# Kernel optimization log

Measured on AMD Instinct MI355X. Metric: run time of the kernel, lower is better.

Reference implementation:

```python
import jax, jax.numpy as jnp
import numpy as np

D_MODEL = 1024
NUM_HEADS = 16
HEAD_DIM = D_MODEL // NUM_HEADS
B, S = 2, 2048


def setup_inputs() -> dict:
    key = jax.random.key(0)
    ks = jax.random.split(key, 6)
    scale = 0.02
    return {
        "x": jax.random.normal(ks[0], (B, S, D_MODEL), dtype=jnp.float32),
        "mask": jax.random.normal(ks[1], (S, S), dtype=jnp.float32),
        "Wqkv": jax.random.normal(ks[2], (D_MODEL, 3 * D_MODEL), dtype=jnp.float32) * scale,
        "bqkv": jax.random.normal(ks[3], (3 * D_MODEL,), dtype=jnp.float32) * scale,
        "Wout": jax.random.normal(ks[4], (D_MODEL, D_MODEL), dtype=jnp.float32) * scale,
        "bout": jax.random.normal(ks[5], (D_MODEL,), dtype=jnp.float32) * scale,
    }


def reference(x, mask, Wqkv, bqkv, Wout, bout):
    b, s, d = x.shape
    h, hd = NUM_HEADS, HEAD_DIM
    qkv = x @ Wqkv + bqkv                              # [b, s, 3d]
    qkv = qkv.reshape(b, s, h, 3 * hd).transpose(0, 2, 1, 3)  # [b, h, s, 3hd]
    q, k, v = jnp.split(qkv, 3, axis=-1)               # each [b, h, s, hd]
    scaled = jnp.einsum("bhqd,bhkd->bhqk", q, k) / jnp.sqrt(jnp.float32(hd))
    scaled = scaled + mask                             # mask [s, s] broadcasts
    attn = jax.nn.softmax(scaled, axis=-1)
    values = jnp.einsum("bhqk,bhkd->bhqd", attn, v)    # [b, h, s, hd]
    values = values.transpose(0, 2, 1, 3).reshape(b, s, d)
    return values @ Wout + bout
```

## Files before the change

kernel.cpp:

```cpp
#include <hip/hip_runtime.h>
#include <hip/hip_bf16.h>

#define D_MODEL 1024
#define NH 16
#define HD 64
#define BATCH 2
#define SEQ 2048
#define M_TOTAL (BATCH*SEQ)

typedef _Float16 f16;
typedef _Float16 half8 __attribute__((ext_vector_type(8)));
typedef _Float16 half4v __attribute__((ext_vector_type(4)));
typedef float floatx4 __attribute__((ext_vector_type(4)));

__device__ inline void gload_lds16(const void* g, void* l) {
    __builtin_amdgcn_global_load_lds(
        (const __attribute__((address_space(1))) unsigned int*)g,
        (__attribute__((address_space(3))) unsigned int*)l, 16, 0, 0);
}

__global__ void cvt_f32_f16(const float* __restrict__ src, f16* __restrict__ dst, int n4) {
    int i = blockIdx.x * blockDim.x + threadIdx.x;
    if (i < n4) {
        float4 v = ((const float4*)src)[i];
        half4v o = { (f16)v.x, (f16)v.y, (f16)v.z, (f16)v.w };
        *(half4v*)(dst + (long)i * 4) = o;
    }
}

__global__ void exp_cvt(const float* __restrict__ src, f16* __restrict__ dst, int n4) {
    int i = blockIdx.x * blockDim.x + threadIdx.x;
    if (i < n4) {
        float4 v = ((const float4*)src)[i];
        half4v o = { (f16)__expf(v.x), (f16)__expf(v.y), (f16)__expf(v.z), (f16)__expf(v.w) };
        *(half4v*)(dst + (long)i * 4) = o;
    }
}

__global__ void transpose_cvt(const float* __restrict__ src, f16* __restrict__ dst, int R, int C) {
    __shared__ float tile[32][33];
    int tx = threadIdx.x;
    int ty = threadIdx.y;
    int c0 = blockIdx.x * 32;
    int r0 = blockIdx.y * 32;
    for (int yy = 0; yy < 32; yy += 8)
        tile[ty + yy][tx] = src[(long)(r0 + ty + yy) * C + c0 + tx];
    __syncthreads();
    for (int yy = 0; yy < 32; yy += 8)
        dst[(long)(c0 + ty + yy) * R + r0 + tx] = (f16)tile[tx][ty + yy];
}

template<int MODE, int TN>
__global__ __launch_bounds__(256) void gemm_mfma(
    const f16* __restrict__ A, const f16* __restrict__ BT,
    const float* __restrict__ bias,
    f16* __restrict__ Qh, f16* __restrict__ Kh, f16* __restrict__ Vtg,
    float* __restrict__ out, int Kdim)
{
    constexpr int NF = TN / 32;
    __shared__ f16 Ah[128 * 64];
    __shared__ f16 Bh[TN * 64];
    int tid  = threadIdx.x;
    int wid  = tid >> 6;
    int lane = tid & 63;
    int quad = lane >> 4;
    int l16  = lane & 15;
    int m0 = blockIdx.y * 128;
    int n0 = blockIdx.x * TN;
    int mrow = (wid >> 1) * 64;
    int ncol = (wid & 1) * (TN / 2);
    int grow = lane >> 3;
    int gchunk = (lane & 7) ^ (grow & 7);
    int sw0 = ((quad)     ^ (l16 & 7)) * 8;
    int sw1 = ((quad + 4) ^ (l16 & 7)) * 8;

    floatx4 acc[4][NF];
    #pragma unroll
    for (int mb = 0; mb < 4; mb++)
        #pragma unroll
        for (int nb = 0; nb < NF; nb++) acc[mb][nb] = (floatx4){0.f, 0.f, 0.f, 0.f};

    const f16* Abase = A + (long)m0 * Kdim;
    const f16* Bbase = BT + (long)n0 * Kdim;

    for (int k0 = 0; k0 < Kdim; k0 += 64) {
        #pragma unroll
        for (int j = 0; j < 4; j++) {
            int r = j * 32 + wid * 8 + grow;
            gload_lds16(Abase + (long)r * Kdim + k0 + gchunk * 8, &Ah[(j * 32 + wid * 8) * 64]);
        }
        #pragma unroll
        for (int j = 0; j < TN / 32; j++) {
            int r = j * 32 + wid * 8 + grow;
            gload_lds16(Bbase + (long)r * Kdim + k0 + gchunk * 8, &Bh[(j * 32 + wid * 8) * 64]);
        }
        __syncthreads();
        #pragma unroll
        for (int h = 0; h < 2; h++) {
            int sw = h ? sw1 : sw0;
            half8 af[4];
            #pragma unroll
            for (int mb = 0; mb < 4; mb++)
                af[mb] = *(const half8*)&Ah[(mrow + mb * 16 + l16) * 64 + sw];
            #pragma unroll
            for (int nb = 0; nb < NF; nb++) {
                half8 bf = *(const half8*)&Bh[(ncol + nb * 16 + l16) * 64 + sw];
                #pragma unroll
                for (int mb = 0; mb < 4; mb++)
                    acc[mb][nb] = __builtin_amdgcn_mfma_f32_16x16x32_f16(af[mb], bf, acc[mb][nb], 0, 0, 0);
            }
        }
        __syncthreads();
    }

    #pragma unroll
    for (int nb = 0; nb < NF; nb++) {
        int n = n0 + ncol + nb * 16 + l16;
        float bv = bias[n];
        int head = 0, t = 0, d = 0;
        if (MODE == 0) { head = n / 192; int rem = n % 192; t = rem / 64; d = rem % 64; }
        #pragma unroll
        for (int mb = 0; mb < 4; mb++) {
            int mbase = m0 + mrow + mb * 16 + quad * 4;
            if (MODE == 0) {
                int b = mbase >> 11;
                int s = mbase & 2047;
                long bh = b * NH + head;
                if (t == 2) {
                    half4v pack;
                    #pragma unroll
                    for (int r = 0; r < 4; r++) pack[r] = (f16)(acc[mb][nb][r] + bv);
                    *(half4v*)&Vtg[(bh * HD + d) * SEQ + s] = pack;
                } else if (t == 0) {
                    #pragma unroll
                    for (int r = 0; r < 4; r++)
                        Qh[(bh * SEQ + s + r) * HD + d] = (f16)((acc[mb][nb][r] + bv) * 0.125f);
                } else {
                    #pragma unroll
                    for (int r = 0; r < 4; r++)
                        Kh[(bh * SEQ + s + r) * HD + d] = (f16)(acc[mb][nb][r] + bv);
                }
            } else {
                #pragma unroll
                for (int r = 0; r < 4; r++)
                    out[(long)(mbase + r) * D_MODEL + n] = acc[mb][nb][r] + bv;
            }
        }
    }
}

__global__ __launch_bounds__(256) void attn(
    const f16* __restrict__ Qh, const f16* __restrict__ Kh, const f16* __restrict__ Vtg,
    const f16* __restrict__ E, f16* __restrict__ valh)
{
    __shared__ f16 Kl[2][64 * 64];
    __shared__ f16 Vt[2][64 * 64];
    int tid  = threadIdx.x;
    int wid  = tid >> 6;
    int lane = tid & 63;
    int quad = lane >> 4;
    int l16  = lane & 15;
    int bh = blockIdx.y;
    int b  = bh >> 4;
    int h  = bh & 15;
    int q0 = blockIdx.x * 128 + wid * 32;

    int grow = lane >> 3;
    int gpos = lane & 7;
    int l3   = l16 & 7;
    int sw0 = ((quad)     ^ l3) * 8;
    int sw1 = ((quad + 4) ^ l3) * 8;
    int qh  = quad >> 1;
    int ql4 = (quad & 1) * 4;

    const f16* Qbase = Qh + ((long)bh * SEQ + q0) * HD;
    half8 qf[2][2];
    #pragma unroll
    for (int m = 0; m < 2; m++)
        #pragma unroll
        for (int c = 0; c < 2; c++)
            qf[m][c] = *(const half8*)&Qbase[(long)(m * 16 + l16) * HD + c * 32 + quad * 8];

    floatx4 Of[2][4];
    float sums[2] = {0.f, 0.f};
    #pragma unroll
    for (int m = 0; m < 2; m++)
        #pragma unroll
        for (int nb = 0; nb < 4; nb++) Of[m][nb] = (floatx4){0.f, 0.f, 0.f, 0.f};

    const f16* Kb = Kh + (long)bh * SEQ * HD;
    const f16* Vb = Vtg + (long)bh * HD * SEQ;

    #pragma unroll
    for (int j = 0; j < 2; j++) {
        int rb = j * 32 + wid * 8;
        int row = rb + grow;
        int gk = gpos ^ (row & 7);
        gload_lds16(Kb + (long)row * HD + gk * 8, &Kl[0][rb * 64]);
        gload_lds16(Vb + (long)row * SEQ + gk * 8, &Vt[0][rb * 64]);
    }

    half4v ef[2][2][4];
    #pragma unroll
    for (int m = 0; m < 2; m++)
        #pragma unroll
        for (int kb = 0; kb < 4; kb++)
            ef[0][m][kb] = *(const half4v*)&E[(long)(q0 + m * 16 + l16) * SEQ + kb * 16 + quad * 4];

    for (int it2 = 0; it2 < SEQ / 128; it2++) {
        #pragma unroll
        for (int p = 0; p < 2; p++) {
            int k0 = it2 * 128 + p * 64;
            __syncthreads();

            if (k0 + 64 < SEQ) {
                int kn = k0 + 64;
                #pragma unroll
                for (int j = 0; j < 2; j++) {
                    int rb = j * 32 + wid * 8;
                    int row = rb + grow;
                    int gk = gpos ^ (row & 7);
                    gload_lds16(Kb + (long)(kn + row) * HD + gk * 8, &Kl[p ^ 1][rb * 64]);
                    gload_lds16(Vb + (long)row * SEQ + kn + gk * 8, &Vt[p ^ 1][rb * 64]);
                }
                #pragma unroll
                for (int m = 0; m < 2; m++)
                    #pragma unroll
                    for (int kb = 0; kb < 4; kb++)
                        ef[p ^ 1][m][kb] = *(const half4v*)&E[(long)(q0 + m * 16 + l16) * SEQ + kn + kb * 16 + quad * 4];
            }

            half4v ph[2][4];
            #pragma unroll
            for (int kb = 0; kb < 4; kb++) {
                half8 kf0 = *(const half8*)&Kl[p][(kb * 16 + l16) * 64 + sw0];
                half8 kf1 = *(const half8*)&Kl[p][(kb * 16 + l16) * 64 + sw1];
                #pragma unroll
                for (int m = 0; m < 2; m++) {
                    floatx4 s = (floatx4){0.f, 0.f, 0.f, 0.f};
                    s = __builtin_amdgcn_mfma_f32_16x16x32_f16(kf0, qf[m][0], s, 0, 0, 0);
                    s = __builtin_amdgcn_mfma_f32_16x16x32_f16(kf1, qf[m][1], s, 0, 0, 0);
                    #pragma unroll
                    for (int r = 0; r < 4; r++) {
                        float pv = (float)ef[p][m][kb][r] * __expf(s[r]);
                        sums[m] += pv;
                        ph[m][kb][r] = (f16)pv;
                    }
                }
            }

            #pragma unroll
            for (int kb = 0; kb < 4; kb++) {
                int chunk = ((kb * 2 + qh) ^ l3) * 8 + ql4;
                #pragma unroll
                for (int nb = 0; nb < 4; nb++) {
                    half4v vf = *(const half4v*)&Vt[p][(nb * 16 + l16) * 64 + chunk];
                    #pragma unroll
                    for (int m = 0; m < 2; m++)
                        Of[m][nb] = __builtin_amdgcn_mfma_f32_16x16x16f16(vf, ph[m][kb], Of[m][nb], 0, 0, 0);
                }
            }
        }
    }

    #pragma unroll
    for (int m = 0; m < 2; m++) {
        float s = sums[m];
        s += __shfl_xor(s, 16);
        s += __shfl_xor(s, 32);
        sums[m] = 1.f / s;
    }

    #pragma unroll
    for (int m = 0; m < 2; m++) {
        long row = (long)(b * SEQ + q0 + m * 16 + l16) * D_MODEL + h * HD;
        #pragma unroll
        for (int nb = 0; nb < 4; nb++) {
            half4v o;
            #pragma unroll
            for (int r = 0; r < 4; r++) o[r] = (f16)(Of[m][nb][r] * sums[m]);
            *(half4v*)&valh[row + nb * 16 + quad * 4] = o;
        }
    }
}

extern "C" void kernel_launch(void* const* d_in, const int* in_sizes, int n_in,
                              void* d_out, int out_size, void* d_ws, size_t ws_size,
                              hipStream_t stream) {
    const float* x    = (const float*)d_in[0];
    const float* mask = (const float*)d_in[1];
    const float* Wqkv = (const float*)d_in[2];
    const float* bqkv = (const float*)d_in[3];
    const float* Wout = (const float*)d_in[4];
    const float* bout = (const float*)d_in[5];
    float* out = (float*)d_out;

    char* ws = (char*)d_ws;
    f16* xh    = (f16*)(ws + 0);
    f16* E     = (f16*)(ws + 0);
    f16* WqkvT = (f16*)(ws + 8388608);
    f16* WoutT = (f16*)(ws + 14680064);
    f16* Qh    = (f16*)(ws + 16777216);
    f16* Kh    = (f16*)(ws + 25165824);
    f16* Vtg   = (f16*)(ws + 33554432);
    f16* valh  = (f16*)(ws + 41943040);

    cvt_f32_f16<<<4096, 256, 0, stream>>>(x, xh, M_TOTAL * D_MODEL / 4);
    transpose_cvt<<<dim3(96, 32), dim3(32, 8), 0, stream>>>(Wqkv, WqkvT, 1024, 3072);
    transpose_cvt<<<dim3(32, 32), dim3(32, 8), 0, stream>>>(Wout, WoutT, 1024, 1024);
    gemm_mfma<0, 128><<<dim3(24, 32), 256, 0, stream>>>(xh, WqkvT, bqkv, Qh, Kh, Vtg, nullptr, 1024);
    exp_cvt<<<4096, 256, 0, stream>>>(mask, E, SEQ * SEQ / 4);
    attn<<<dim3(16, 32), 256, 0, stream>>>(Qh, Kh, Vtg, E, valh);
    gemm_mfma<1, 64><<<dim3(16, 32), 256, 0, stream>>>(valh, WoutT, bout, nullptr, nullptr, nullptr, out, 1024);
}
```

Measured before the change: 243.3 us.

## Shrink attention blocks, use exp2 with folded scale, MFMA row sums

The attention kernel now runs 128-thread blocks over 64 queries with a single K/V LDS buffer, which doubles the grid and raises occupancy. Softmax exponentials use exp2 with log2e folded into the Q scaling. Probabilities are converted and multiplied by the exp-mask in packed fp16. Row sums come from an extra MFMA against a ones vector instead of per-lane adds and shuffles. The double-buffered prefetch of K/V is lost, so load latency must now be hidden by having more resident blocks.

```diff
diff --git a/kernel.cpp b/kernel.cpp
--- a/kernel.cpp
+++ b/kernel.cpp
@@ -11,12 +11,19 @@
 typedef _Float16 f16;
 typedef _Float16 half8 __attribute__((ext_vector_type(8)));
 typedef _Float16 half4v __attribute__((ext_vector_type(4)));
+typedef _Float16 half2v __attribute__((ext_vector_type(2)));
+typedef __fp16 fp16x2 __attribute__((ext_vector_type(2)));
 typedef float floatx4 __attribute__((ext_vector_type(4)));
 
 __device__ inline void gload_lds16(const void* g, void* l) {
     __builtin_amdgcn_global_load_lds(
         (const __attribute__((address_space(1))) unsigned int*)g,
         (__attribute__((address_space(3))) unsigned int*)l, 16, 0, 0);
+}
+
+__device__ inline half2v pack_f16(float a, float b) {
+    fp16x2 t = __builtin_amdgcn_cvt_pkrtz(a, b);
+    return __builtin_bit_cast(half2v, t);
 }
 
 __global__ void cvt_f32_f16(const float* __restrict__ src, f16* __restrict__ dst, int n4) {
@@ -134,7 +141,7 @@
                 } else if (t == 0) {
                     #pragma unroll
                     for (int r = 0; r < 4; r++)
-                        Qh[(bh * SEQ + s + r) * HD + d] = (f16)((acc[mb][nb][r] + bv) * 0.125f);
+                        Qh[(bh * SEQ + s + r) * HD + d] = (f16)((acc[mb][nb][r] + bv) * 0.1803368801f);
                 } else {
                     #pragma unroll
                     for (int r = 0; r < 4; r++)
@@ -149,12 +156,12 @@
     }
 }
 
-__global__ __launch_bounds__(256) void attn(
+__global__ __launch_bounds__(128, 4) void attn(
     const f16* __restrict__ Qh, const f16* __restrict__ Kh, const f16* __restrict__ Vtg,
     const f16* __restrict__ E, f16* __restrict__ valh)
 {
-    __shared__ f16 Kl[2][64 * 64];
-    __shared__ f16 Vt[2][64 * 64];
+    __shared__ f16 Kl[64 * 64];
+    __shared__ f16 Vt[64 * 64];
     int tid  = threadIdx.x;
     int wid  = tid >> 6;
     int lane = tid & 63;
@@ -163,7 +170,7 @@
     int bh = blockIdx.y;
     int b  = bh >> 4;
     int h  = bh & 15;
-    int q0 = blockIdx.x * 128 + wid * 32;
+    int q0 = blockIdx.x * 64 + wid * 32;
 
     int grow = lane >> 3;
     int gpos = lane & 7;
@@ -181,72 +188,80 @@
         for (int c = 0; c < 2; c++)
             qf[m][c] = *(const half8*)&Qbase[(long)(m * 16 + l16) * HD + c * 32 + quad * 8];
 
+    half4v vones;
+    #pragma unroll
+    for (int j = 0; j < 4; j++) vones[j] = (f16)1.0f;
+
     floatx4 Of[2][4];
-    float sums[2] = {0.f, 0.f};
-    #pragma unroll
-    for (int m = 0; m < 2; m++)
+    floatx4 Ofs[2];
+    #pragma unroll
+    for (int m = 0; m < 2; m++) {
+        Ofs[m] = (floatx4){0.f, 0.f, 0.f, 0.f};
         #pragma unroll
         for (int nb = 0; nb < 4; nb++) Of[m][nb] = (floatx4){0.f, 0.f, 0.f, 0.f};
+    }
 
     const f16* Kb = Kh + (long)bh * SEQ * HD;
     const f16* Vb = Vtg + (long)bh * HD * SEQ;
-
-    #pragma unroll
-    for (int j = 0; j < 2; j++) {
-        int rb = j * 32 + wid * 8;
-        int row = rb + grow;
-        int gk = gpos ^ (row & 7);
-        gload_lds16(Kb + (long)row * HD + gk * 8, &Kl[0][rb * 64]);
-        gload_lds16(Vb + (long)row * SEQ + gk * 8, &Vt[0][rb * 64]);
-    }
+    const f16* Erow0 = E + (long)(q0 + l16) * SEQ + quad * 4;
+    const f16* Erow1 = E + (long)(q0 + 16 + l16) * SEQ + quad * 4;
 
     half4v ef[2][2][4];
     #pragma unroll
-    for (int m = 0; m < 2; m++)
-        #pragma unroll
-        for (int kb = 0; kb < 4; kb++)
-            ef[0][m][kb] = *(const half4v*)&E[(long)(q0 + m * 16 + l16) * SEQ + kb * 16 + quad * 4];
+    for (int kb = 0; kb < 4; kb++) {
+        ef[0][0][kb] = *(const half4v*)&Erow0[kb * 16];
+        ef[0][1][kb] = *(const half4v*)&Erow1[kb * 16];
+    }
 
     for (int it2 = 0; it2 < SEQ / 128; it2++) {
         #pragma unroll
         for (int p = 0; p < 2; p++) {
-            int k0 = it2 * 128 + p * 64;
+            int k0 = (it2 * 2 + p) * 64;
+            __syncthreads();
+            #pragma unroll
+            for (int j = 0; j < 4; j++) {
+                int rb = wid * 32 + j * 8;
+                int row = rb + grow;
+                int gk = gpos ^ grow;
+                gload_lds16(Kb + (long)(k0 + row) * HD + gk * 8, &Kl[rb * 64]);
+                gload_lds16(Vb + (long)row * SEQ + k0 + gk * 8, &Vt[rb * 64]);
+            }
             __syncthreads();
 
             if (k0 + 64 < SEQ) {
                 int kn = k0 + 64;
                 #pragma unroll
-                for (int j = 0; j < 2; j++) {
-                    int rb = j * 32 + wid * 8;
-                    int row = rb + grow;
-                    int gk = gpos ^ (row & 7);
-                    gload_lds16(Kb + (long)(kn + row) * HD + gk * 8, &Kl[p ^ 1][rb * 64]);
-                    gload_lds16(Vb + (long)row * SEQ + kn + gk * 8, &Vt[p ^ 1][rb * 64]);
+                for (int kb = 0; kb < 4; kb++) {
+                    ef[p ^ 1][0][kb] = *(const half4v*)&Erow0[kn + kb * 16];
+                    ef[p ^ 1][1][kb] = *(const half4v*)&Erow1[kn + kb * 16];
                 }
-                #pragma unroll
-                for (int m = 0; m < 2; m++)
-                    #pragma unroll
-                    for (int kb = 0; kb < 4; kb++)
-                        ef[p ^ 1][m][kb] = *(const half4v*)&E[(long)(q0 + m * 16 + l16) * SEQ + kn + kb * 16 + quad * 4];
             }
 
             half4v ph[2][4];
             #pragma unroll
             for (int kb = 0; kb < 4; kb++) {
-                half8 kf0 = *(const half8*)&Kl[p][(kb * 16 + l16) * 64 + sw0];
-                half8 kf1 = *(const half8*)&Kl[p][(kb * 16 + l16) * 64 + sw1];
+                half8 kf0 = *(const half8*)&Kl[(kb * 16 + l16) * 64 + sw0];
+                half8 kf1 = *(const half8*)&Kl[(kb * 16 + l16) * 64 + sw1];
                 #pragma unroll
                 for (int m = 0; m < 2; m++) {
                     floatx4 s = (floatx4){0.f, 0.f, 0.f, 0.f};
                     s = __builtin_amdgcn_mfma_f32_16x16x32_f16(kf0, qf[m][0], s, 0, 0, 0);
                     s = __builtin_amdgcn_mfma_f32_16x16x32_f16(kf1, qf[m][1], s, 0, 0, 0);
-                    #pragma unroll
-                    for (int r = 0; r < 4; r++) {
-                        float pv = (float)ef[p][m][kb][r] * __expf(s[r]);
-                        sums[m] += pv;
-                        ph[m][kb][r] = (f16)pv;
-                    }
+                    half2v lo = pack_f16(__builtin_amdgcn_exp2f(s[0]), __builtin_amdgcn_exp2f(s[1]));
+                    half2v hi = pack_f16(__builtin_amdgcn_exp2f(s[2]), __builtin_amdgcn_exp2f(s[3]));
+                    half2v el = { ef[p][m][kb][0], ef[p][m][kb][1] };
+                    half2v eh = { ef[p][m][kb][2], ef[p][m][kb][3] };
+                    lo *= el;
+                    hi *= eh;
+                    half4v pp = { lo[0], lo[1], hi[0], hi[1] };
+                    ph[m][kb] = pp;
                 }
+            }
+
+            #pragma unroll
+            for (int kb = 0; kb < 4; kb++) {
+                Ofs[0] = __builtin_amdgcn_mfma_f32_16x16x16f16(vones, ph[0][kb], Ofs[0], 0, 0, 0);
+                Ofs[1] = __builtin_amdgcn_mfma_f32_16x16x16f16(vones, ph[1][kb], Ofs[1], 0, 0, 0);
             }
 
             #pragma unroll
@@ -254,7 +269,7 @@
                 int chunk = ((kb * 2 + qh) ^ l3) * 8 + ql4;
                 #pragma unroll
                 for (int nb = 0; nb < 4; nb++) {
-                    half4v vf = *(const half4v*)&Vt[p][(nb * 16 + l16) * 64 + chunk];
+                    half4v vf = *(const half4v*)&Vt[(nb * 16 + l16) * 64 + chunk];
                     #pragma unroll
                     for (int m = 0; m < 2; m++)
                         Of[m][nb] = __builtin_amdgcn_mfma_f32_16x16x16f16(vf, ph[m][kb], Of[m][nb], 0, 0, 0);
@@ -263,13 +278,9 @@
         }
     }
 
-    #pragma unroll
-    for (int m = 0; m < 2; m++) {
-        float s = sums[m];
-        s += __shfl_xor(s, 16);
-        s += __shfl_xor(s, 32);
-        sums[m] = 1.f / s;
-    }
+    float rs[2];
+    #pragma unroll
+    for (int m = 0; m < 2; m++) rs[m] = 1.f / Ofs[m][0];
 
     #pragma unroll
     for (int m = 0; m < 2; m++) {
@@ -278,7 +289,7 @@
         for (int nb = 0; nb < 4; nb++) {
             half4v o;
             #pragma unroll
-            for (int r = 0; r < 4; r++) o[r] = (f16)(Of[m][nb][r] * sums[m]);
+            for (int r = 0; r < 4; r++) o[r] = (f16)(Of[m][nb][r] * rs[m]);
             *(half4v*)&valh[row + nb * 16 + quad * 4] = o;
         }
     }
@@ -310,6 +321,6 @@
     transpose_cvt<<<dim3(32, 32), dim3(32, 8), 0, stream>>>(Wout, WoutT, 1024, 1024);
     gemm_mfma<0, 128><<<dim3(24, 32), 256, 0, stream>>>(xh, WqkvT, bqkv, Qh, Kh, Vtg, nullptr, 1024);
     exp_cvt<<<4096, 256, 0, stream>>>(mask, E, SEQ * SEQ / 4);
-    attn<<<dim3(16, 32), 256, 0, stream>>>(Qh, Kh, Vtg, E, valh);
+    attn<<<dim3(32, 32), 128, 0, stream>>>(Qh, Kh, Vtg, E, valh);
     gemm_mfma<1, 64><<<dim3(16, 32), 256, 0, stream>>>(valh, WoutT, bout, nullptr, nullptr, nullptr, out, 1024);
 }
```

Result: slower. 308.1 us (+26.6%).
